# Kernel tuning notes

Measured on AMD Instinct MI355X. Metric: run time of the kernel, lower is better.

The kernel has to match this reference:

```python
import jax, jax.numpy as jnp
import numpy as np

GRID = 128          # voxel grid extent per axis
KERNELS = [2, 4, 8] # kernel_size == stride pooling scales
B = 4               # number of batches (point clouds)


def _pool_unpool(feats, seg, num_seg):
    # avg-pool over segment then broadcast back to original points
    sums = jax.ops.segment_sum(feats, seg, num_segments=num_seg)
    cnts = jax.ops.segment_sum(jnp.ones((feats.shape[0], 1), feats.dtype), seg, num_segments=num_seg)
    means = sums / jnp.maximum(cnts, 1.0)
    return means[seg]


def setup_inputs() -> dict:
    key = jax.random.key(0)
    k1, k2, k3, k4, k5 = jax.random.split(key, 5)
    N, C, OUT = 1_048_576, 64, 96
    mult = len(KERNELS) + 1
    feats = jax.random.normal(k1, (N, C), jnp.float32)
    coords = jax.random.randint(k2, (N, 3), 0, GRID, jnp.int32)
    batch_idx = jax.random.randint(k3, (N,), 0, B, jnp.int32)
    W = jax.random.normal(k4, (OUT, C * mult), jnp.float32) / np.sqrt(C * mult)
    b = jax.random.normal(k5, (OUT,), jnp.float32) * 0.01
    return {"feats": feats, "coords": coords, "batch_idx": batch_idx, "W": W, "b": b}


def reference(feats, coords, batch_idx, W, b):
    bidx = batch_idx.astype(jnp.int32)
    # i == 0: global average pooling per batch + MinkowskiBroadcast back to points
    cat = [_pool_unpool(feats, bidx, B)]
    # pyramid levels: AvgPool(k, stride=k) then PoolingTranspose(k, stride=k)
    for k in KERNELS:
        s = GRID // k  # pooled grid size per axis
        pc = coords // k
        seg = ((bidx * s + pc[:, 0]) * s + pc[:, 1]) * s + pc[:, 2]
        cat.append(_pool_unpool(feats, seg, B * s * s * s))
    out = jnp.concatenate(cat, axis=1)  # [N, C * (len(KERNELS)+1)]
    return out @ W.T + b                # MinkowskiLinear
```

## Files before the change

### kernel.cpp

```cpp
#include <hip/hip_runtime.h>
#include <stdint.h>


#define N_PTS   1048576
#define NB      4
#define N2SEG   (NB*64*64*64)
#define N4SEG   (NB*32*32*32)
#define N8SEG   (NB*16*16*16)

typedef unsigned int uint;

#define OFF_SUMS2  ((size_t)0)
#define OFF_CNT2   ((size_t)134217728)
#define OFF_SUMS0F ((size_t)138412032)
#define ZERO_BEG   OFF_CNT2
#define ZERO_END   ((size_t)138413056)
#define OFF_SUMS4  ((size_t)138413056)
#define OFF_MEAN4  ((size_t)155190272)
#define OFF_CNT4   ((size_t)171967488)
#define OFF_SUMS8  ((size_t)172491776)
#define OFF_MEAN8  ((size_t)174588928)
#define OFF_CNT8   ((size_t)176686080)
#define OFF_MEAN0  ((size_t)176751616)
#define OFF_WF     ((size_t)176752640)
#define WS_NEEDED  ((size_t)176801792)

#define D_S2 0u
#define D_C2 ((uint)(OFF_CNT2 / 4))
#define D_M4 ((uint)(OFF_MEAN4 / 4))
#define D_M8 ((uint)(OFF_MEAN8 / 4))
#define D_M0 ((uint)(OFF_MEAN0 / 4))

typedef short s8v __attribute__((ext_vector_type(8)));
typedef float f4v __attribute__((ext_vector_type(4)));
typedef uint  u4v __attribute__((ext_vector_type(4)));
typedef float f2v __attribute__((ext_vector_type(2)));

__device__ __forceinline__ uint pack_bf16x2(float a, float b) {
  uint ua = __float_as_uint(a), ub = __float_as_uint(b);
  ua = (ua + 0x7fffu + ((ua >> 16) & 1u)) >> 16;
  ub = (ub + 0x7fffu + ((ub >> 16) & 1u)) >> 16;
  return (ub << 16) | ua;
}
__device__ __forceinline__ float bflo(uint u) { return __uint_as_float(u << 16); }
__device__ __forceinline__ float bfhi(uint u) { return __uint_as_float(u & 0xffff0000u); }

__device__ __forceinline__ uint scale_pk(uint u, float rc) {
  return pack_bf16x2(bflo(u) * rc, bfhi(u) * rc);
}

#define ZCNT_U4 ((ZERO_END - ZERO_BEG) / 16)
__global__ __launch_bounds__(256) void k_zero_cnt(u4v* __restrict__ p) {
  u4v z = (u4v)0u;
  size_t stride = (size_t)gridDim.x * 256;
  for (size_t i = blockIdx.x * 256ull + threadIdx.x; i < ZCNT_U4; i += stride)
    __builtin_nontemporal_store(z, &p[i]);
}

__global__ __launch_bounds__(256) void k_cnt(
    const int* __restrict__ coords, const int* __restrict__ batch,
    uint* __restrict__ cnt2)
{
  int p = blockIdx.x * 256 + threadIdx.x;
  int b = batch[p];
  int x = coords[3 * p], y = coords[3 * p + 1], z = coords[3 * p + 2];
  int s2 = ((b * 64 + (x >> 1)) * 64 + (y >> 1)) * 64 + (z >> 1);
  atomicAdd(&cnt2[s2], 1u);
}

__global__ __launch_bounds__(256) void k_zmulti(
    const uint* __restrict__ cnt2, u4v* __restrict__ sums2q)
{
  int tid = blockIdx.x * 256 + threadIdx.x;
  int seg = tid >> 3, part = tid & 7;
  if (cnt2[seg] >= 2u) sums2q[seg * 8 + part] = (u4v)0u;
}

__global__ __launch_bounds__(256) void k_wf(const float* __restrict__ W,
                                            uint* __restrict__ Wf) {
  int idx = blockIdx.x * 256 + threadIdx.x;
  int d = idx & 3, l = (idx >> 2) & 63, ktnt = idx >> 8;
  int kt = ktnt / 6, nt = ktnt - kt * 6;
  int n = nt * 16 + (l & 15);
  int k = kt * 32 + (l >> 4) * 8 + d * 2;
  Wf[idx] = pack_bf16x2(W[n * 256 + k], W[n * 256 + k + 1]);
}

__global__ __launch_bounds__(256) void k_scatter2(
    const float* __restrict__ feats, const int* __restrict__ coords,
    const int* __restrict__ batch, uint* __restrict__ sums2,
    const uint* __restrict__ cnt2)
{
  int l = threadIdx.x & 63;
  int c2 = l & 31, half = l >> 5;
  int wid = (blockIdx.x * 256 + threadIdx.x) >> 6;
  int nw = (gridDim.x * 256) >> 6;
  for (int p0 = wid * 2; p0 < N_PTS; p0 += nw * 2) {
    int p = p0 + half;
    f2v f = __builtin_nontemporal_load(((const f2v*)feats) + (size_t)p * 32 + c2);
    int b = batch[p];
    int x = coords[3 * p], y = coords[3 * p + 1], z = coords[3 * p + 2];
    int s2 = ((b * 64 + (x >> 1)) * 64 + (y >> 1)) * 64 + (z >> 1);
    uint pk = pack_bf16x2(f.x, f.y);
    uint cv = cnt2[s2];
    uint* dst = sums2 + (size_t)s2 * 32 + c2;
    if (cv == 1u) {
      *dst = pk;
    } else {
      uint64_t addr = (uint64_t)(uintptr_t)dst;
      asm volatile("global_atomic_pk_add_bf16 %0, %1, off"
                   :: "v"(addr), "v"(pk));
    }
  }
}

__global__ __launch_bounds__(256) void k_down_bf(
    const uint* __restrict__ sumsF, const uint* __restrict__ cntF,
    uint* __restrict__ sumsC, uint* __restrict__ meanC,
    uint* __restrict__ cntC, int lgC, int nC)
{
  int tid = blockIdx.x * 256 + threadIdx.x;
  int sc = tid >> 5, c2 = tid & 31;
  if (sc >= nC) return;
  int CG = 1 << lgC, FG = CG << 1;
  int b = sc >> (3 * lgC);
  int r = sc & ((1 << (3 * lgC)) - 1);
  int x = r >> (2 * lgC), y = (r >> lgC) & (CG - 1), z = r & (CG - 1);
  float sx = 0.f, sy = 0.f;
  uint cn = 0;
  #pragma unroll
  for (int dx = 0; dx < 2; ++dx)
    #pragma unroll
    for (int dy = 0; dy < 2; ++dy)
      #pragma unroll
      for (int dz = 0; dz < 2; ++dz) {
        int sf = ((b * FG + 2 * x + dx) * FG + (2 * y + dy)) * FG + (2 * z + dz);
        uint cf = cntF[sf];
        if (cf) {
          uint u = sumsF[(size_t)sf * 32 + c2];
          sx += bflo(u); sy += bfhi(u);
        }
        cn += cf;
      }
  sumsC[(size_t)sc * 32 + c2] = pack_bf16x2(sx, sy);
  float rc = 1.0f / (float)(cn > 1u ? cn : 1u);
  meanC[(size_t)sc * 32 + c2] = pack_bf16x2(sx * rc, sy * rc);
  if (c2 == 0) cntC[sc] = cn;
}

__global__ __launch_bounds__(256) void k_gpart(
    const uint* __restrict__ sums8, float* __restrict__ sums0f)
{
  __shared__ float2 red[8][32];
  int b = blockIdx.x >> 5, chunk = blockIdx.x & 31;
  int t = threadIdx.x, c2 = t & 31, g = t >> 5;
  float sx = 0.f, sy = 0.f;
  for (int i = g; i < 128; i += 8) {
    uint u = sums8[(size_t)(b * 4096 + chunk * 128 + i) * 32 + c2];
    sx += bflo(u); sy += bfhi(u);
  }
  red[g][c2] = make_float2(sx, sy);
  __syncthreads();
  if (g == 0) {
    float ax = 0.f, ay = 0.f;
    #pragma unroll
    for (int i = 0; i < 8; ++i) { ax += red[i][c2].x; ay += red[i][c2].y; }
    unsafeAtomicAdd(&sums0f[b * 64 + 2 * c2], ax);
    unsafeAtomicAdd(&sums0f[b * 64 + 2 * c2 + 1], ay);
  }
}

__global__ __launch_bounds__(256) void k_fin0(
    const float* __restrict__ sums0f, const uint* __restrict__ cnt8,
    uint* __restrict__ mean0)
{
  __shared__ uint redc[256];
  __shared__ float rcs[NB];
  int t = threadIdx.x;
  uint cn = 0;
  for (int i = 0; i < 64; ++i) cn += cnt8[t * 64 + i];
  redc[t] = cn;
  __syncthreads();
  if (t < NB) {
    uint s = 0;
    for (int i = 0; i < 64; ++i) s += redc[t * 64 + i];
    rcs[t] = 1.0f / (float)(s > 1u ? s : 1u);
  }
  __syncthreads();
  if (t < 128) {
    int b = t >> 5, c2 = t & 31;
    float rc = rcs[b];
    mean0[b * 32 + c2] =
        pack_bf16x2(sums0f[b * 64 + 2 * c2] * rc, sums0f[b * 64 + 2 * c2 + 1] * rc);
  }
}

#define GPB 8
__global__ __launch_bounds__(256) void k_final(
    const int* __restrict__ coords, const int* __restrict__ batch,
    const uint* __restrict__ wsb,
    const uint4* __restrict__ Wf, const float* __restrict__ bias,
    float* __restrict__ out)
{
  __shared__ uint4 wf[3072];
  int t = threadIdx.x;
  #pragma unroll
  for (int i = 0; i < 12; ++i) wf[i * 256 + t] = Wf[i * 256 + t];
  int l = t & 63, w = t >> 6, pl = l & 15, q = l >> 4;
  float bn[6];
  #pragma unroll
  for (int nt = 0; nt < 6; ++nt) bn[nt] = bias[nt * 16 + pl];
  __syncthreads();

  uint4 afc[8];
  uint cvc;
  {
    int p = blockIdx.x * (GPB * 64) + w * 16 + pl;
    int b = batch[p];
    int x = coords[3 * p], y = coords[3 * p + 1], z = coords[3 * p + 2];
    int s2 = ((b * 64 + (x >> 1)) * 64 + (y >> 1)) * 64 + (z >> 1);
    int s4 = ((b * 32 + (x >> 2)) * 32 + (y >> 2)) * 32 + (z >> 2);
    int s8 = ((b * 16 + (x >> 3)) * 16 + (y >> 3)) * 16 + (z >> 3);
    const uint4* a0 = (const uint4*)(wsb + D_M0 + b * 32);
    const uint4* a2 = (const uint4*)(wsb + D_S2 + s2 * 32);
    const uint4* a4 = (const uint4*)(wsb + D_M4 + s4 * 32);
    const uint4* a8 = (const uint4*)(wsb + D_M8 + s8 * 32);
    afc[0] = a0[q];     afc[1] = a0[4 + q];
    afc[2] = a2[q];     afc[3] = a2[4 + q];
    afc[4] = a4[q];     afc[5] = a4[4 + q];
    afc[6] = a8[q];     afc[7] = a8[4 + q];
    cvc = wsb[D_C2 + s2];
  }

  #pragma unroll 1
  for (int g = 0; g < GPB; ++g) {
    uint4 afn[8];
    uint cvn = 0;
    if (g + 1 < GPB) {
      int p = blockIdx.x * (GPB * 64) + (g + 1) * 64 + w * 16 + pl;
      int b = batch[p];
      int x = coords[3 * p], y = coords[3 * p + 1], z = coords[3 * p + 2];
      int s2 = ((b * 64 + (x >> 1)) * 64 + (y >> 1)) * 64 + (z >> 1);
      int s4 = ((b * 32 + (x >> 2)) * 32 + (y >> 2)) * 32 + (z >> 2);
      int s8 = ((b * 16 + (x >> 3)) * 16 + (y >> 3)) * 16 + (z >> 3);
      const uint4* a0 = (const uint4*)(wsb + D_M0 + b * 32);
      const uint4* a2 = (const uint4*)(wsb + D_S2 + s2 * 32);
      const uint4* a4 = (const uint4*)(wsb + D_M4 + s4 * 32);
      const uint4* a8 = (const uint4*)(wsb + D_M8 + s8 * 32);
      afn[0] = a0[q];     afn[1] = a0[4 + q];
      afn[2] = a2[q];     afn[3] = a2[4 + q];
      afn[4] = a4[q];     afn[5] = a4[4 + q];
      afn[6] = a8[q];     afn[7] = a8[4 + q];
      cvn = wsb[D_C2 + s2];
    }

    float rc = 1.0f / (float)(cvc > 1u ? cvc : 1u);
    afc[2].x = scale_pk(afc[2].x, rc); afc[2].y = scale_pk(afc[2].y, rc);
    afc[2].z = scale_pk(afc[2].z, rc); afc[2].w = scale_pk(afc[2].w, rc);
    afc[3].x = scale_pk(afc[3].x, rc); afc[3].y = scale_pk(afc[3].y, rc);
    afc[3].z = scale_pk(afc[3].z, rc); afc[3].w = scale_pk(afc[3].w, rc);
    f4v acc[6];
    #pragma unroll
    for (int nt = 0; nt < 6; ++nt) acc[nt] = (f4v)0.0f;
    #pragma unroll
    for (int kt = 0; kt < 8; ++kt) {
      s8v afr = __builtin_bit_cast(s8v, afc[kt]);
      #pragma unroll
      for (int nt = 0; nt < 6; ++nt) {
        s8v bf = __builtin_bit_cast(s8v, wf[(kt * 6 + nt) * 64 + l]);
        acc[nt] = __builtin_amdgcn_mfma_f32_16x16x32_bf16(afr, bf, acc[nt], 0, 0, 0);
      }
    }
    int pbase = blockIdx.x * (GPB * 64) + g * 64 + w * 16;
    float* ob = out + (size_t)(pbase + q * 4) * 96 + pl;
    #pragma unroll
    for (int nt = 0; nt < 6; ++nt)
      #pragma unroll
      for (int r = 0; r < 4; ++r)
        ob[r * 96 + nt * 16] = bn[nt] + acc[nt][r];

    #pragma unroll
    for (int i = 0; i < 8; ++i) afc[i] = afn[i];
    cvc = cvn;
  }
}

extern "C" void kernel_launch(void* const* d_in, const int* in_sizes, int n_in,
                              void* d_out, int out_size, void* d_ws, size_t ws_size,
                              hipStream_t stream)
{
  const float* feats  = (const float*)d_in[0];
  const int*   coords = (const int*)d_in[1];
  const int*   batch  = (const int*)d_in[2];
  const float* W      = (const float*)d_in[3];
  const float* bias   = (const float*)d_in[4];
  float* out = (float*)d_out;
  char* ws = (char*)d_ws;
  if (ws_size < WS_NEEDED) return;

  uint*  sums2  = (uint*)(ws + OFF_SUMS2);
  uint*  cnt2   = (uint*)(ws + OFF_CNT2);
  float* sums0f = (float*)(ws + OFF_SUMS0F);
  uint*  sums4  = (uint*)(ws + OFF_SUMS4);
  uint*  mean4  = (uint*)(ws + OFF_MEAN4);
  uint*  cnt4   = (uint*)(ws + OFF_CNT4);
  uint*  sums8  = (uint*)(ws + OFF_SUMS8);
  uint*  mean8  = (uint*)(ws + OFF_MEAN8);
  uint*  cnt8   = (uint*)(ws + OFF_CNT8);
  uint*  mean0  = (uint*)(ws + OFF_MEAN0);
  uint*  Wf     = (uint*)(ws + OFF_WF);

  k_wf<<<48, 256, 0, stream>>>(W, Wf);
  k_zero_cnt<<<1024, 256, 0, stream>>>((u4v*)(ws + ZERO_BEG));
  k_cnt<<<N_PTS / 256, 256, 0, stream>>>(coords, batch, cnt2);
  k_zmulti<<<(N2SEG * 8) / 256, 256, 0, stream>>>(cnt2, (u4v*)sums2);
  k_scatter2<<<8192, 256, 0, stream>>>(feats, coords, batch, sums2, cnt2);
  k_down_bf<<<(N4SEG * 32) / 256, 256, 0, stream>>>(sums2, cnt2, sums4, mean4, cnt4, 5, N4SEG);
  k_down_bf<<<(N8SEG * 32) / 256, 256, 0, stream>>>(sums4, cnt4, sums8, mean8, cnt8, 4, N8SEG);
  k_gpart<<<128, 256, 0, stream>>>(sums8, sums0f);
  k_fin0<<<1, 256, 0, stream>>>(sums0f, cnt8, mean0);
  k_final<<<N_PTS / (GPB * 64), 256, 0, stream>>>(
      coords, batch, (const uint*)ws, (const uint4*)Wf, bias, out);
}
```

Measured before the change: 419.0 us.

## Precompute segment indices in LDS and triple-buffer gathers in final GEMM kernel

The final kernel now computes all segment indices for its 512 points up front with coalesced loads and stores them packed in shared memory. The per-group loop is fully unrolled with three register buffers, so each gather is issued two groups ahead of its MFMA consumption instead of one. This hides more of the random-gather latency and moves index math off the critical path. In exchange it raises register pressure, which may reduce occupancy.

```diff
diff --git a/kernel.cpp b/kernel.cpp
--- a/kernel.cpp
+++ b/kernel.cpp
@@ -196,6 +196,46 @@
 }
 
 #define GPB 8
+
+#define ISSUE(G, AF, CV) {                                                   \
+    uint2 iv = idx_lds[(G) * 64 + w16pl];                                    \
+    const uint4* a2 = (const uint4*)(wsb + D_S2 + iv.x * 32u);               \
+    const uint4* a4 = (const uint4*)(wsb + D_M4 + (iv.y & 0x1FFFFu) * 32u);  \
+    const uint4* a8 = (const uint4*)(wsb + D_M8 + (iv.y >> 17) * 32u);       \
+    const uint4* a0 = (const uint4*)(wsb + D_M0 + (iv.y >> 29) * 32u);       \
+    AF[0] = a0[q];  AF[1] = a0[4 + q];                                       \
+    AF[2] = a2[q];  AF[3] = a2[4 + q];                                       \
+    AF[4] = a4[q];  AF[5] = a4[4 + q];                                       \
+    AF[6] = a8[q];  AF[7] = a8[4 + q];                                       \
+    CV = wsb[D_C2 + iv.x];                                                   \
+  }
+
+#define CONSUME(G, AF, CV) {                                                 \
+    float rc = 1.0f / (float)(CV > 1u ? CV : 1u);                            \
+    AF[2].x = scale_pk(AF[2].x, rc); AF[2].y = scale_pk(AF[2].y, rc);        \
+    AF[2].z = scale_pk(AF[2].z, rc); AF[2].w = scale_pk(AF[2].w, rc);        \
+    AF[3].x = scale_pk(AF[3].x, rc); AF[3].y = scale_pk(AF[3].y, rc);        \
+    AF[3].z = scale_pk(AF[3].z, rc); AF[3].w = scale_pk(AF[3].w, rc);        \
+    f4v acc[6];                                                              \
+    _Pragma("unroll")                                                        \
+    for (int nt = 0; nt < 6; ++nt) acc[nt] = (f4v)0.0f;                      \
+    _Pragma("unroll")                                                        \
+    for (int kt = 0; kt < 8; ++kt) {                                         \
+      s8v afr = __builtin_bit_cast(s8v, AF[kt]);                             \
+      _Pragma("unroll")                                                      \
+      for (int nt = 0; nt < 6; ++nt) {                                       \
+        s8v bf = __builtin_bit_cast(s8v, wf[(kt * 6 + nt) * 64 + l]);        \
+        acc[nt] = __builtin_amdgcn_mfma_f32_16x16x32_bf16(afr, bf, acc[nt], 0, 0, 0); \
+      }                                                                      \
+    }                                                                        \
+    float* ob = out + (size_t)(pb + (G) * 64 + w * 16 + q * 4) * 96 + pl;    \
+    _Pragma("unroll")                                                        \
+    for (int nt = 0; nt < 6; ++nt)                                           \
+      _Pragma("unroll")                                                      \
+      for (int r = 0; r < 4; ++r)                                            \
+        ob[r * 96 + nt * 16] = bn[nt] + acc[nt][r];                          \
+  }
+
 __global__ __launch_bounds__(256) void k_final(
     const int* __restrict__ coords, const int* __restrict__ batch,
     const uint* __restrict__ wsb,
@@ -203,86 +243,41 @@
     float* __restrict__ out)
 {
   __shared__ uint4 wf[3072];
+  __shared__ uint2 idx_lds[512];
   int t = threadIdx.x;
   #pragma unroll
   for (int i = 0; i < 12; ++i) wf[i * 256 + t] = Wf[i * 256 + t];
+  int pb = blockIdx.x * (GPB * 64);
+  #pragma unroll
+  for (int j = 0; j < 2; ++j) {
+    int pi = t + j * 256;
+    int p = pb + pi;
+    int b = batch[p];
+    int x = coords[3 * p], y = coords[3 * p + 1], z = coords[3 * p + 2];
+    uint s2 = (uint)(((b * 64 + (x >> 1)) * 64 + (y >> 1)) * 64 + (z >> 1));
+    uint s4 = (uint)(((b * 32 + (x >> 2)) * 32 + (y >> 2)) * 32 + (z >> 2));
+    uint s8 = (uint)(((b * 16 + (x >> 3)) * 16 + (y >> 3)) * 16 + (z >> 3));
+    idx_lds[pi] = make_uint2(s2, s4 | (s8 << 17));
+  }
   int l = t & 63, w = t >> 6, pl = l & 15, q = l >> 4;
+  int w16pl = w * 16 + pl;
   float bn[6];
   #pragma unroll
   for (int nt = 0; nt < 6; ++nt) bn[nt] = bias[nt * 16 + pl];
   __syncthreads();
 
-  uint4 afc[8];
-  uint cvc;
-  {
-    int p = blockIdx.x * (GPB * 64) + w * 16 + pl;
-    int b = batch[p];
-    int x = coords[3 * p], y = coords[3 * p + 1], z = coords[3 * p + 2];
-    int s2 = ((b * 64 + (x >> 1)) * 64 + (y >> 1)) * 64 + (z >> 1);
-    int s4 = ((b * 32 + (x >> 2)) * 32 + (y >> 2)) * 32 + (z >> 2);
-    int s8 = ((b * 16 + (x >> 3)) * 16 + (y >> 3)) * 16 + (z >> 3);
-    const uint4* a0 = (const uint4*)(wsb + D_M0 + b * 32);
-    const uint4* a2 = (const uint4*)(wsb + D_S2 + s2 * 32);
-    const uint4* a4 = (const uint4*)(wsb + D_M4 + s4 * 32);
-    const uint4* a8 = (const uint4*)(wsb + D_M8 + s8 * 32);
-    afc[0] = a0[q];     afc[1] = a0[4 + q];
-    afc[2] = a2[q];     afc[3] = a2[4 + q];
-    afc[4] = a4[q];     afc[5] = a4[4 + q];
-    afc[6] = a8[q];     afc[7] = a8[4 + q];
-    cvc = wsb[D_C2 + s2];
-  }
-
-  #pragma unroll 1
-  for (int g = 0; g < GPB; ++g) {
-    uint4 afn[8];
-    uint cvn = 0;
-    if (g + 1 < GPB) {
-      int p = blockIdx.x * (GPB * 64) + (g + 1) * 64 + w * 16 + pl;
-      int b = batch[p];
-      int x = coords[3 * p], y = coords[3 * p + 1], z = coords[3 * p + 2];
-      int s2 = ((b * 64 + (x >> 1)) * 64 + (y >> 1)) * 64 + (z >> 1);
-      int s4 = ((b * 32 + (x >> 2)) * 32 + (y >> 2)) * 32 + (z >> 2);
-      int s8 = ((b * 16 + (x >> 3)) * 16 + (y >> 3)) * 16 + (z >> 3);
-      const uint4* a0 = (const uint4*)(wsb + D_M0 + b * 32);
-      const uint4* a2 = (const uint4*)(wsb + D_S2 + s2 * 32);
-      const uint4* a4 = (const uint4*)(wsb + D_M4 + s4 * 32);
-      const uint4* a8 = (const uint4*)(wsb + D_M8 + s8 * 32);
-      afn[0] = a0[q];     afn[1] = a0[4 + q];
-      afn[2] = a2[q];     afn[3] = a2[4 + q];
-      afn[4] = a4[q];     afn[5] = a4[4 + q];
-      afn[6] = a8[q];     afn[7] = a8[4 + q];
-      cvn = wsb[D_C2 + s2];
-    }
-
-    float rc = 1.0f / (float)(cvc > 1u ? cvc : 1u);
-    afc[2].x = scale_pk(afc[2].x, rc); afc[2].y = scale_pk(afc[2].y, rc);
-    afc[2].z = scale_pk(afc[2].z, rc); afc[2].w = scale_pk(afc[2].w, rc);
-    afc[3].x = scale_pk(afc[3].x, rc); afc[3].y = scale_pk(afc[3].y, rc);
-    afc[3].z = scale_pk(afc[3].z, rc); afc[3].w = scale_pk(afc[3].w, rc);
-    f4v acc[6];
-    #pragma unroll
-    for (int nt = 0; nt < 6; ++nt) acc[nt] = (f4v)0.0f;
-    #pragma unroll
-    for (int kt = 0; kt < 8; ++kt) {
-      s8v afr = __builtin_bit_cast(s8v, afc[kt]);
-      #pragma unroll
-      for (int nt = 0; nt < 6; ++nt) {
-        s8v bf = __builtin_bit_cast(s8v, wf[(kt * 6 + nt) * 64 + l]);
-        acc[nt] = __builtin_amdgcn_mfma_f32_16x16x32_bf16(afr, bf, acc[nt], 0, 0, 0);
-      }
-    }
-    int pbase = blockIdx.x * (GPB * 64) + g * 64 + w * 16;
-    float* ob = out + (size_t)(pbase + q * 4) * 96 + pl;
-    #pragma unroll
-    for (int nt = 0; nt < 6; ++nt)
-      #pragma unroll
-      for (int r = 0; r < 4; ++r)
-        ob[r * 96 + nt * 16] = bn[nt] + acc[nt][r];
-
-    #pragma unroll
-    for (int i = 0; i < 8; ++i) afc[i] = afn[i];
-    cvc = cvn;
-  }
+  uint4 b0[8], b1[8], b2[8];
+  uint c0, c1, c2v;
+  ISSUE(0, b0, c0)
+  ISSUE(1, b1, c1)
+  ISSUE(2, b2, c2v)  CONSUME(0, b0, c0)
+  ISSUE(3, b0, c0)   CONSUME(1, b1, c1)
+  ISSUE(4, b1, c1)   CONSUME(2, b2, c2v)
+  ISSUE(5, b2, c2v)  CONSUME(3, b0, c0)
+  ISSUE(6, b0, c0)   CONSUME(4, b1, c1)
+  ISSUE(7, b1, c1)   CONSUME(5, b2, c2v)
+  CONSUME(6, b0, c0)
+  CONSUME(7, b1, c1)
 }
 
 extern "C" void kernel_launch(void* const* d_in, const int* in_sizes, int n_in,
```

After: 411.5 us. Within noise of the previous version (-1.8%).
